# Optimization experiments

Hardware: AMD Instinct MI355X
Metric: run time of the kernel (lower is better)

Reference implementation:

```python
import jax, jax.numpy as jnp
import numpy as np

B, T, A, C = 16, 100, 3, 80
GRIDS = (128, 64, 32)
IGNORE = -100


def setup_inputs() -> dict:
    key = jax.random.key(0)
    k0, k1, k2, kc, kx, kv = jax.random.split(key, 6)
    out0 = jax.random.normal(k0, (B, A, GRIDS[0], GRIDS[0], 5 + C), dtype=jnp.float32)
    out1 = jax.random.normal(k1, (B, A, GRIDS[1], GRIDS[1], 5 + C), dtype=jnp.float32)
    out2 = jax.random.normal(k2, (B, A, GRIDS[2], GRIDS[2], 5 + C), dtype=jnp.float32)
    cls = jax.random.randint(kc, (B, T), 0, C).astype(jnp.float32)
    xy = jax.random.uniform(kx, (B, T, 2), minval=0.01, maxval=0.99, dtype=jnp.float32)
    # rows that are all-zero are padding (filtered by the original loop)
    valid = jax.random.uniform(kv, (B, T)) < 0.6
    valid = valid.at[:, 0].set(True)  # ensure >=1 target per image (torch CE would NaN otherwise)
    targets = jnp.concatenate([cls[..., None], xy, jnp.zeros((B, T, 2), jnp.float32)], axis=-1)
    targets = targets * valid[..., None].astype(jnp.float32)
    return {"out0": out0, "out1": out1, "out2": out2, "targets": targets}


def _scale_loss(output, targets):
    # output: [B, A, H, W, 5+C]
    _, nA, H, W, c5 = output.shape
    nC = c5 - 5

    def per_b(out_b, tgt_b):
        valid = ~jnp.all(tgt_b == 0.0, axis=1)            # [T]
        rows = (tgt_b[:, 2] * H).astype(jnp.int32)        # y*h, truncation == torch .long()
        cols = (tgt_b[:, 1] * W).astype(jnp.int32)        # x*w
        rows = jnp.where(valid, rows, H)                  # invalid -> OOB -> dropped scatter
        cls_id = tgt_b[:, 0].astype(jnp.int32)
        gt = jnp.full((H, W), IGNORE, dtype=jnp.int32)
        gt = gt.at[rows, cols].set(cls_id, mode="drop")  # index_put_
        # NB: original repeats gt over anchors in (H, W, A) order while prediction is
        # flattened in (A, H, W) order; we faithfully reproduce that pairing.
        gt_flat = jnp.broadcast_to(gt[:, :, None], (H, W, nA)).reshape(-1)   # [H*W*A]
        pred = out_b[..., 5:].reshape(-1, nC)                                 # [A*H*W, C]
        logp = jax.nn.log_softmax(pred, axis=-1)
        mask = gt_flat != IGNORE
        safe = jnp.where(mask, gt_flat, 0)
        nll = -jnp.take_along_axis(logp, safe[:, None], axis=1)[:, 0]
        denom = jnp.maximum(jnp.sum(mask), 1)
        return jnp.sum(jnp.where(mask, nll, 0.0)) / denom  # CE mean over non-ignored

    return jnp.sum(jax.vmap(per_b)(output, targets))


def reference(out0, out1, out2, targets):
    loss = _scale_loss(out0, targets) + _scale_loss(out1, targets) + _scale_loss(out2, targets)
    return loss / out2.shape[0]  # divided by batch_size of the last scale
```

## Files before the change

### kernel.cpp

```cpp
#include <hip/hip_runtime.h>
#include <math.h>

#define NT 100
#define NA 3
#define NC 80
#define NSCALE 3
#define NB 16
#define CH 8
#define NPART (NB * NSCALE * CH)

__global__ __launch_bounds__(256) void class_loss_kernel(
    const float* __restrict__ out0,
    const float* __restrict__ out1,
    const float* __restrict__ out2,
    const float* __restrict__ targets,
    float* __restrict__ partials)
{
    const int bs    = blockIdx.x / CH;
    const int chunk = blockIdx.x % CH;
    const int b = bs / NSCALE;
    const int s = bs % NSCALE;

    const float* out;
    int H;
    if (s == 0)      { out = out0; H = 128; }
    else if (s == 1) { out = out1; H = 64;  }
    else             { out = out2; H = 32;  }
    const int W = H;
    const int HW = H * W;

    __shared__ int   s_cell[NT];
    __shared__ int   s_cls[NT];
    __shared__ int   s_wcell[NT];
    __shared__ int   s_wcls[NT];
    __shared__ int   s_cnt[2];
    __shared__ float s_wavesum[4];

    const int tid  = threadIdx.x;
    const int wave = tid >> 6;
    const int lane = tid & 63;

    if (tid < NT) {
        const float* tg = targets + ((size_t)b * NT + tid) * 5;
        float c  = tg[0];
        float x  = tg[1];
        float y  = tg[2];
        float z3 = tg[3];
        float z4 = tg[4];
        bool valid = (c != 0.0f) || (x != 0.0f) || (y != 0.0f) ||
                     (z3 != 0.0f) || (z4 != 0.0f);
        int cell = -1, cls = 0;
        if (valid) {
            int row = (int)(y * (float)H);
            int col = (int)(x * (float)W);
            cell = row * W + col;
            cls  = (int)c;
        }
        s_cell[tid] = cell;
        s_cls[tid]  = cls;
    }
    __syncthreads();

    int  mycell = (tid < NT) ? s_cell[tid] : -1;
    bool win    = (tid < NT) && (mycell >= 0);
    #pragma unroll 4
    for (int u = 0; u < NT; ++u) {
        int cu = s_cell[u];
        win = win && !((u > tid) && (cu == mycell));
    }
    unsigned long long m = __ballot(win);
    if (wave < 2 && lane == 0) s_cnt[wave] = __popcll(m);
    __syncthreads();

    if (win) {
        int pos = __popcll(m & ((1ull << lane) - 1ull));
        if (wave == 1) pos += s_cnt[0];
        s_wcell[pos] = mycell;
        s_wcls[pos]  = s_cls[tid];
    }
    __syncthreads();

    const int n      = s_cnt[0] + s_cnt[1];
    const int ntasks = n * NA;
    const int gw     = chunk * 4 + wave;

    float acc = 0.0f;
    for (int task = gw; task < ntasks; task += 4 * CH) {
        int wi   = task / NA;
        int a    = task - wi * NA;
        int cell = s_wcell[wi];
        int cls  = s_wcls[wi];

        int i = cell * NA + a;
        int a2  = i / HW;
        int rem = i - a2 * HW;
        int h2  = rem / W;
        int w2  = rem - h2 * W;

        const float* base =
            out + ((((size_t)b * NA + a2) * H + h2) * (size_t)W + w2) * (5 + NC) + 5;

        float x0 = base[lane];
        float x1 = (lane < 16) ? base[64 + lane] : -INFINITY;

        float mx = fmaxf(x0, x1);
        #pragma unroll
        for (int off = 32; off; off >>= 1) mx = fmaxf(mx, __shfl_xor(mx, off));

        float e = __builtin_expf(x0 - mx) +
                  ((lane < 16) ? __builtin_expf(x1 - mx) : 0.0f);
        #pragma unroll
        for (int off = 32; off; off >>= 1) e += __shfl_xor(e, off);

        float logsum = mx + __builtin_logf(e);

        float xt = (cls < 64) ? __shfl(x0, cls) : __shfl(x1, cls - 64);
        acc += (logsum - xt);
    }

    if (lane == 0) s_wavesum[wave] = acc;
    __syncthreads();

    if (tid == 0) {
        float total = s_wavesum[0] + s_wavesum[1] + s_wavesum[2] + s_wavesum[3];
        int denom = ntasks > 0 ? ntasks : 1;
        partials[blockIdx.x] = total / (float)denom;
    }
}

__global__ __launch_bounds__(128) void reduce_kernel(
    const float* __restrict__ partials, float* __restrict__ out)
{
    __shared__ float sm[128];
    const int tid = threadIdx.x;
    float a = partials[tid] + partials[tid + 128] + partials[tid + 256];
    sm[tid] = a;
    __syncthreads();
    #pragma unroll
    for (int off = 64; off; off >>= 1) {
        if (tid < off) sm[tid] += sm[tid + off];
        __syncthreads();
    }
    if (tid == 0) out[0] = sm[0] / (float)NB;
}

extern "C" void kernel_launch(void* const* d_in, const int* in_sizes, int n_in,
                              void* d_out, int out_size, void* d_ws, size_t ws_size,
                              hipStream_t stream) {
    const float* out0    = (const float*)d_in[0];
    const float* out1    = (const float*)d_in[1];
    const float* out2    = (const float*)d_in[2];
    const float* targets = (const float*)d_in[3];

    float* partials = (float*)d_ws;
    float* loss     = (float*)d_out;

    class_loss_kernel<<<NPART, 256, 0, stream>>>(out0, out1, out2, targets, partials);
    reduce_kernel<<<1, 128, 0, stream>>>(partials, loss);
}
```

Before: 20.46 us.

## Assign fixed target-anchor tasks per wave and prefetch logits before dedup

Each wave now owns up to two fixed (target, anchor) slots across 38 blocks per batch-scale, instead of looping over a compacted winner list. The logit loads are issued before the O(NT) duplicate-cell scan and ballot, so memory latency overlaps with the dedup work. Non-winning or invalid targets are masked out when accumulating, and the compaction pass with its extra barrier is removed. The price is many more blocks, loads of unused rows for padding targets, and a larger final reduction.

```diff
diff --git a/kernel.cpp b/kernel.cpp
--- a/kernel.cpp
+++ b/kernel.cpp
@@ -6,8 +6,8 @@
 #define NC 80
 #define NSCALE 3
 #define NB 16
-#define CH 8
-#define NPART (NB * NSCALE * CH)
+#define BPB 38
+#define NBLK (NB * NSCALE * BPB)
 
 __global__ __launch_bounds__(256) void class_loss_kernel(
     const float* __restrict__ out0,
@@ -16,24 +16,20 @@
     const float* __restrict__ targets,
     float* __restrict__ partials)
 {
-    const int bs    = blockIdx.x / CH;
-    const int chunk = blockIdx.x % CH;
+    const int bs = blockIdx.x / BPB;
+    const int j  = blockIdx.x % BPB;
     const int b = bs / NSCALE;
     const int s = bs % NSCALE;
 
-    const float* out;
-    int H;
+    const float* out; int H;
     if (s == 0)      { out = out0; H = 128; }
     else if (s == 1) { out = out1; H = 64;  }
     else             { out = out2; H = 32;  }
-    const int W = H;
-    const int HW = H * W;
+    const int W = H, HW = H * W;
 
-    __shared__ int   s_cell[NT];
-    __shared__ int   s_cls[NT];
-    __shared__ int   s_wcell[NT];
-    __shared__ int   s_wcls[NT];
-    __shared__ int   s_cnt[2];
+    __shared__ int s_cell[NT];
+    __shared__ int s_cls[NT];
+    __shared__ unsigned long long s_mask[2];
     __shared__ float s_wavesum[4];
 
     const int tid  = threadIdx.x;
@@ -42,18 +38,12 @@
 
     if (tid < NT) {
         const float* tg = targets + ((size_t)b * NT + tid) * 5;
-        float c  = tg[0];
-        float x  = tg[1];
-        float y  = tg[2];
-        float z3 = tg[3];
-        float z4 = tg[4];
-        bool valid = (c != 0.0f) || (x != 0.0f) || (y != 0.0f) ||
-                     (z3 != 0.0f) || (z4 != 0.0f);
+        float c = tg[0], x = tg[1], y = tg[2], z3 = tg[3], z4 = tg[4];
+        bool valid = (c != 0.f) || (x != 0.f) || (y != 0.f) ||
+                     (z3 != 0.f) || (z4 != 0.f);
         int cell = -1, cls = 0;
         if (valid) {
-            int row = (int)(y * (float)H);
-            int col = (int)(x * (float)W);
-            cell = row * W + col;
+            cell = (int)(y * (float)H) * W + (int)(x * (float)W);
             cls  = (int)c;
         }
         s_cell[tid] = cell;
@@ -61,61 +51,72 @@
     }
     __syncthreads();
 
+    const int t0 = j * 4 + wave;
+    const int t1 = t0 + 4 * BPB;
+    const bool have1 = (t1 < NT * NA);
+
+    const int wi0 = t0 / NA, a0 = t0 - wi0 * NA;
+    const int wi1 = have1 ? (t1 / NA) : 0;
+    const int a1  = have1 ? (t1 - wi1 * NA) : 0;
+
+    const int cell0 = s_cell[wi0], cls0 = s_cls[wi0];
+    const int cell1 = s_cell[wi1], cls1 = s_cls[wi1];
+
+    const int c0 = (cell0 >= 0) ? cell0 : 0;
+    const int i0 = c0 * NA + a0;
+    const int A0 = i0 / HW, r0 = i0 - A0 * HW;
+    const float* base0 = out + (((size_t)b * NA + A0) * HW + r0) * (5 + NC) + 5;
+
+    const int c1 = (cell1 >= 0) ? cell1 : 0;
+    const int i1 = c1 * NA + a1;
+    const int A1 = i1 / HW, r1 = i1 - A1 * HW;
+    const float* base1 = out + (((size_t)b * NA + A1) * HW + r1) * (5 + NC) + 5;
+
+    float x00 = base0[lane];
+    float x01 = (lane < 16) ? base0[64 + lane] : -INFINITY;
+    float x10 = base1[lane];
+    float x11 = (lane < 16) ? base1[64 + lane] : -INFINITY;
+
     int  mycell = (tid < NT) ? s_cell[tid] : -1;
-    bool win    = (tid < NT) && (mycell >= 0);
+    bool win    = (mycell >= 0);
     #pragma unroll 4
     for (int u = 0; u < NT; ++u) {
         int cu = s_cell[u];
-        win = win && !((u > tid) && (cu == mycell));
+        if (u > tid && cu == mycell) win = false;
     }
-    unsigned long long m = __ballot(win);
-    if (wave < 2 && lane == 0) s_cnt[wave] = __popcll(m);
+    unsigned long long mb = __ballot(win);
+    if (wave < 2 && lane == 0) s_mask[wave] = mb;
     __syncthreads();
 
-    if (win) {
-        int pos = __popcll(m & ((1ull << lane) - 1ull));
-        if (wave == 1) pos += s_cnt[0];
-        s_wcell[pos] = mycell;
-        s_wcls[pos]  = s_cls[tid];
-    }
-    __syncthreads();
-
-    const int n      = s_cnt[0] + s_cnt[1];
-    const int ntasks = n * NA;
-    const int gw     = chunk * 4 + wave;
+    const unsigned long long m0 = s_mask[0], m1 = s_mask[1];
+    const int n = __popcll(m0) + __popcll(m1);
+    const bool w0 = (wi0 < 64) ? ((m0 >> wi0) & 1ull) : ((m1 >> (wi0 - 64)) & 1ull);
+    const bool w1 = (wi1 < 64) ? ((m0 >> wi1) & 1ull) : ((m1 >> (wi1 - 64)) & 1ull);
 
     float acc = 0.0f;
-    for (int task = gw; task < ntasks; task += 4 * CH) {
-        int wi   = task / NA;
-        int a    = task - wi * NA;
-        int cell = s_wcell[wi];
-        int cls  = s_wcls[wi];
-
-        int i = cell * NA + a;
-        int a2  = i / HW;
-        int rem = i - a2 * HW;
-        int h2  = rem / W;
-        int w2  = rem - h2 * W;
-
-        const float* base =
-            out + ((((size_t)b * NA + a2) * H + h2) * (size_t)W + w2) * (5 + NC) + 5;
-
-        float x0 = base[lane];
-        float x1 = (lane < 16) ? base[64 + lane] : -INFINITY;
-
-        float mx = fmaxf(x0, x1);
+    {
+        float mx = fmaxf(x00, x01);
         #pragma unroll
         for (int off = 32; off; off >>= 1) mx = fmaxf(mx, __shfl_xor(mx, off));
-
-        float e = __builtin_expf(x0 - mx) +
-                  ((lane < 16) ? __builtin_expf(x1 - mx) : 0.0f);
+        float e = __builtin_expf(x00 - mx) +
+                  ((lane < 16) ? __builtin_expf(x01 - mx) : 0.0f);
         #pragma unroll
         for (int off = 32; off; off >>= 1) e += __shfl_xor(e, off);
-
         float logsum = mx + __builtin_logf(e);
-
-        float xt = (cls < 64) ? __shfl(x0, cls) : __shfl(x1, cls - 64);
-        acc += (logsum - xt);
+        float xt = (cls0 < 64) ? __shfl(x00, cls0) : __shfl(x01, cls0 - 64);
+        if (cell0 >= 0 && w0) acc += (logsum - xt);
+    }
+    if (have1) {
+        float mx = fmaxf(x10, x11);
+        #pragma unroll
+        for (int off = 32; off; off >>= 1) mx = fmaxf(mx, __shfl_xor(mx, off));
+        float e = __builtin_expf(x10 - mx) +
+                  ((lane < 16) ? __builtin_expf(x11 - mx) : 0.0f);
+        #pragma unroll
+        for (int off = 32; off; off >>= 1) e += __shfl_xor(e, off);
+        float logsum = mx + __builtin_logf(e);
+        float xt = (cls1 < 64) ? __shfl(x10, cls1) : __shfl(x11, cls1 - 64);
+        if (cell1 >= 0 && w1) acc += (logsum - xt);
     }
 
     if (lane == 0) s_wavesum[wave] = acc;
@@ -123,21 +124,25 @@
 
     if (tid == 0) {
         float total = s_wavesum[0] + s_wavesum[1] + s_wavesum[2] + s_wavesum[3];
-        int denom = ntasks > 0 ? ntasks : 1;
-        partials[blockIdx.x] = total / (float)denom;
+        partials[blockIdx.x] = total / (float)(n * NA);
     }
 }
 
-__global__ __launch_bounds__(128) void reduce_kernel(
+__global__ __launch_bounds__(256) void reduce_kernel(
     const float* __restrict__ partials, float* __restrict__ out)
 {
-    __shared__ float sm[128];
+    __shared__ float sm[256];
     const int tid = threadIdx.x;
-    float a = partials[tid] + partials[tid + 128] + partials[tid + 256];
+    float a = 0.0f;
+    #pragma unroll
+    for (int k = 0; k < (NBLK + 255) / 256; ++k) {
+        int idx = tid + k * 256;
+        if (idx < NBLK) a += partials[idx];
+    }
     sm[tid] = a;
     __syncthreads();
     #pragma unroll
-    for (int off = 64; off; off >>= 1) {
+    for (int off = 128; off; off >>= 1) {
         if (tid < off) sm[tid] += sm[tid + off];
         __syncthreads();
     }
@@ -155,6 +160,6 @@
     float* partials = (float*)d_ws;
     float* loss     = (float*)d_out;
 
-    class_loss_kernel<<<NPART, 256, 0, stream>>>(out0, out1, out2, targets, partials);
-    reduce_kernel<<<1, 128, 0, stream>>>(partials, loss);
+    class_loss_kernel<<<NBLK, 256, 0, stream>>>(out0, out1, out2, targets, partials);
+    reduce_kernel<<<1, 256, 0, stream>>>(partials, loss);
 }
```

New measurement: 19.00 us. 1.08x faster.
